# Kernel tuning notes

Hardware: AMD Instinct MI355X
Metric: run time of the kernel (lower is better)

## Reference

```python
import jax, jax.numpy as jnp
import numpy as np

DIM = 25
N_NODES = 20000
N_EDGES = 320000
NFEAT = 300
NHID = 64
NCLASS = 50


def setup_inputs() -> dict:
    key = jax.random.key(0)
    ks = jax.random.split(key, 8)
    s1 = np.sqrt(6.0 / (NFEAT + NHID))
    s2 = np.sqrt(6.0 / (NHID * DIM + NCLASS))
    return {
        "x": jax.random.normal(ks[0], (N_NODES, NFEAT), dtype=jnp.float32),
        "adj_rows": jax.random.randint(ks[1], (DIM, N_EDGES), 0, N_NODES, dtype=jnp.int32),
        "adj_cols": jax.random.randint(ks[2], (DIM, N_EDGES), 0, N_NODES, dtype=jnp.int32),
        "adj_vals": jax.random.uniform(ks[3], (DIM, N_EDGES), dtype=jnp.float32),
        "W1": jax.random.uniform(ks[4], (DIM, NFEAT, NHID), dtype=jnp.float32, minval=-s1, maxval=s1),
        "b1": jnp.zeros((DIM, NHID), dtype=jnp.float32),
        "W2": jax.random.uniform(ks[5], (DIM, NHID * DIM, NCLASS), dtype=jnp.float32, minval=-s2, maxval=s2),
        "b2": jnp.zeros((DIM, NCLASS), dtype=jnp.float32),
    }


def _spmm(rows, cols, vals, sup, n):
    # sparse [n,n] @ dense [n,f] via gather + segment-sum scatter-add
    return jax.ops.segment_sum(vals[:, None] * sup[cols], rows, num_segments=n)


def reference(x, adj_rows, adj_cols, adj_vals, W1, b1, W2, b2):
    n = x.shape[0]
    spmm = jax.vmap(lambda r, c, v, s: _spmm(r, c, v, s, n))
    # layer 1: per-branch dense mm, spmm, bias, relu  -> [DIM, n, NHID]
    sup1 = jnp.einsum("nf,dfh->dnh", x, W1)
    h1 = jax.nn.relu(spmm(adj_rows, adj_cols, adj_vals, sup1) + b1[:, None, :])
    # permute + reshape: concat branch features per node -> [n, DIM*NHID]
    h1cat = jnp.transpose(h1, (1, 0, 2)).reshape(n, -1)
    # layer 2: per-branch dense mm, spmm, bias, relu -> [DIM, n, NCLASS]
    sup2 = jnp.einsum("nk,dkc->dnc", h1cat, W2)
    h2 = jax.nn.relu(spmm(adj_rows, adj_cols, adj_vals, sup2) + b2[:, None, :])
    # max-pool over branches (POOLING='max')
    return jnp.max(h2, axis=0)
```

## Files before the change

### kernel.cpp

```cpp
#include <hip/hip_runtime.h>
#include <hip/hip_bf16.h>
#include <cstdint>
#include <cstddef>

#define DIM 25
#define NN 20000
#define NE 320000
#define NF 300
#define NH 64
#define NC 50
#define K2 (DIM*NH)
#define KP1 320
#define B1T_ROWS 1664
#define B2T_ROWS 1280
#define NBK 79
#define EPB 4096
#define BPB ((NE + EPB - 1) / EPB)
#define FCAP 5632

typedef __attribute__((ext_vector_type(8))) short short8;
typedef __attribute__((ext_vector_type(4))) float floatx4;
typedef __hip_bfloat16 bf16;

static __device__ __forceinline__ unsigned bf16bits(float f) {
    bf16 b = __float2bfloat16(f);
    return (unsigned)*reinterpret_cast<unsigned short*>(&b);
}
static __device__ __forceinline__ float blo(unsigned w) { return __uint_as_float(w << 16); }
static __device__ __forceinline__ float bhi(unsigned w) { return __uint_as_float(w & 0xFFFF0000u); }

static __device__ __forceinline__ void gld16(const void* g, void* l) {
    __builtin_amdgcn_global_load_lds((const __attribute__((address_space(1))) unsigned*)g,
                                     (__attribute__((address_space(3))) unsigned*)l, 16, 0, 0);
}

__global__ void zero_kernel(int* __restrict__ p, int n) {
    int i = blockIdx.x * blockDim.x + threadIdx.x;
    if (i < n) p[i] = 0;
}

__global__ __launch_bounds__(256) void bucket_scatter_kernel(const int* __restrict__ rows,
                                                             const int* __restrict__ cols,
                                                             const float* __restrict__ vals,
                                                             int* __restrict__ gcur,
                                                             unsigned* __restrict__ interE,
                                                             unsigned char* __restrict__ interR) {
    const int d = blockIdx.y;
    const int e0 = blockIdx.x * EPB;
    __shared__ int lh[NBK];
    __shared__ int lo[NBK];
    __shared__ int lbase[NBK];
    __shared__ unsigned entE[EPB];
    __shared__ unsigned short entR[EPB];
    const int tid = threadIdx.x;
    for (int i = tid; i < NBK; i += 256) lh[i] = 0;
    __syncthreads();
    const int* rd = rows + (size_t)d * NE;
    const int* cd = cols + (size_t)d * NE;
    const float* vd = vals + (size_t)d * NE;
    const int e1 = min(e0 + EPB, NE);
    const int ne = e1 - e0;
    for (int i = e0 + tid; i < e1; i += 256)
        atomicAdd(&lh[rd[i] >> 8], 1);
    __syncthreads();
    if (tid == 0) {
        int run = 0;
        for (int b = 0; b < NBK; ++b) { lo[b] = run; run += lh[b]; }
    }
    __syncthreads();
    for (int i = tid; i < NBK; i += 256) {
        lbase[i] = lh[i] ? atomicAdd(&gcur[d * NBK + i], lh[i]) : 0;
        lh[i] = 0;
    }
    __syncthreads();
    for (int i = e0 + tid; i < e1; i += 256) {
        int r = rd[i];
        int b = r >> 8;
        int rank = atomicAdd(&lh[b], 1);
        int pos = lo[b] + rank;
        entE[pos] = (unsigned)cd[i] | (bf16bits(vd[i]) << 16);
        entR[pos] = (unsigned short)r;
    }
    __syncthreads();
    for (int p = tid; p < ne; p += 256) {
        int r = entR[p];
        int b = r >> 8;
        int gpos = lbase[b] + (p - lo[b]);
        if (gpos < FCAP) {
            size_t slot = ((size_t)d * NBK + b) * FCAP + gpos;
            interE[slot] = entE[p];
            interR[slot] = (unsigned char)r;
        }
    }
}

__global__ void bucket_scan_kernel(const int* __restrict__ gcur,
                                   int* __restrict__ offs_b,
                                   int* __restrict__ bcnt,
                                   int* __restrict__ offs) {
    const int d = blockIdx.x;
    if (threadIdx.x != 0) return;
    int run = 0;
    for (int b = 0; b < NBK; ++b) {
        int c = min(gcur[d * NBK + b], FCAP);
        offs_b[d * NBK + b] = run;
        bcnt[d * NBK + b] = c;
        run += c;
    }
    offs[d * (NN + 1) + NN] = run;
}

__global__ __launch_bounds__(256) void csr_finalize_kernel(const unsigned* __restrict__ interE,
                                                           const unsigned char* __restrict__ interR,
                                                           const int* __restrict__ offs_b,
                                                           const int* __restrict__ bcnt,
                                                           int* __restrict__ offs,
                                                           unsigned* __restrict__ sedge) {
    const int d = blockIdx.y;
    const int b = blockIdx.x;
    const int tid = threadIdx.x;
    const int s = offs_b[d * NBK + b];
    const int cnt = bcnt[d * NBK + b];
    const size_t base = ((size_t)d * NBK + b) * FCAP;
    __shared__ int sm[256];
    __shared__ int cur[256];
    __shared__ unsigned lse[FCAP];
    sm[tid] = 0;
    __syncthreads();
    for (int i = tid; i < cnt; i += 256)
        atomicAdd(&sm[interR[base + i]], 1);
    __syncthreads();
    int own = sm[tid];
    for (int off = 1; off < 256; off <<= 1) {
        int t = (tid >= off) ? sm[tid - off] : 0;
        __syncthreads();
        sm[tid] += t;
        __syncthreads();
    }
    int excl = sm[tid] - own;
    int row = (b << 8) + tid;
    if (row < NN) offs[d * (NN + 1) + row] = s + excl;
    cur[tid] = excl;
    __syncthreads();
    for (int i = tid; i < cnt; i += 256) {
        int idx = atomicAdd(&cur[interR[base + i]], 1);
        lse[idx] = interE[base + i];
    }
    __syncthreads();
    unsigned* sed = sedge + (size_t)d * NE;
    for (int t = tid; t < cnt; t += 256)
        sed[s + t] = lse[t];
}

__global__ void pack_x_kernel(const float* __restrict__ x, bf16* __restrict__ xb) {
    int i = blockIdx.x * blockDim.x + threadIdx.x;
    if (i >= NN * KP1) return;
    int n = i / KP1, k = i - n * KP1;
    xb[i] = __float2bfloat16((k < NF) ? x[(size_t)n * NF + k] : 0.f);
}

__global__ void pack_b1_kernel(const float* __restrict__ W1, bf16* __restrict__ b1t) {
    int i = blockIdx.x * blockDim.x + threadIdx.x;
    if (i >= B1T_ROWS * KP1) return;
    int j2 = i / KP1, k = i - j2 * KP1;
    int chunk = j2 >> 9;
    int r = j2 & 511;
    int d = chunk * 8 + (r >> 6);
    float v = 0.f;
    if (d < DIM && k < NF)
        v = W1[(size_t)d * NF * NH + (size_t)k * NH + (r & 63)];
    b1t[i] = __float2bfloat16(v);
}

__global__ void pack_b2_kernel(const float* __restrict__ W2, bf16* __restrict__ b2t) {
    int i = blockIdx.x * blockDim.x + threadIdx.x;
    if (i >= B2T_ROWS * K2) return;
    int r = i / K2, k = i - r * K2;
    float v = 0.f;
    if (r < DIM * NC) {
        int g = r / NC, c = r - g * NC;
        v = W2[(size_t)g * K2 * NC + (size_t)k * NC + c];
    }
    b2t[i] = __float2bfloat16(v);
}

__global__ __launch_bounds__(256) void gemm_bf16_kernel(const bf16* __restrict__ A, int lda,
                                                        const bf16* __restrict__ BT, int ldb,
                                                        bf16* __restrict__ C,
                                                        int ksteps, int mode, int nvalid) {
    __shared__ unsigned short As[3 * 128 * 32];
    __shared__ unsigned short Bs[3 * 128 * 32];
    const int tid = threadIdx.x;
    const int wave = tid >> 6;
    const int lane = tid & 63;

    const int mtiles = (int)gridDim.x;
    const int ntiles = (int)gridDim.y;
    const int bid = (int)blockIdx.y * mtiles + (int)blockIdx.x;
    const int per_group = 8 * ntiles;
    const int group = bid / per_group;
    const int rem = bid - group * per_group;
    const int first_m = group * 8;
    const int gm = min(8, mtiles - first_m);
    const int mt = first_m + rem % gm;
    const int nt = rem / gm;
    const int m0 = mt * 128;
    const int n0 = nt * 128;

    const int wm = (wave >> 1) * 64;
    const int wn = (wave & 1) * 64;
    floatx4 acc[4][4] = {};
    const int r0 = tid >> 2;
    const int cg = (tid & 3) ^ ((r0 >> 1) & 3);
    const int q8 = (lane >> 4) * 8;
    const int gq = q8 >> 3;
    unsigned short* lA0 = As + wave * 512;
    unsigned short* lA1 = As + 2048 + wave * 512;
    unsigned short* lB0 = Bs + wave * 512;
    unsigned short* lB1 = Bs + 2048 + wave * 512;
    const bf16* gA0 = A + (size_t)(m0 + r0) * lda + cg * 8;
    const bf16* gA1 = A + (size_t)(m0 + r0 + 64) * lda + cg * 8;
    const bf16* gB0 = BT + (size_t)(n0 + r0) * ldb + cg * 8;
    const bf16* gB1 = BT + (size_t)(n0 + r0 + 64) * ldb + cg * 8;

    int offA[4], offB[4];
    #pragma unroll
    for (int i = 0; i < 4; ++i) {
        int ra = wm + i * 16 + (lane & 15);
        int rb = wn + i * 16 + (lane & 15);
        offA[i] = ra * 32 + ((gq ^ ((ra >> 1) & 3)) << 3);
        offB[i] = rb * 32 + ((gq ^ ((rb >> 1) & 3)) << 3);
    }

    gld16(gA0, lA0); gld16(gA1, lA1); gld16(gB0, lB0); gld16(gB1, lB1);
    if (ksteps > 1) {
        gld16(gA0 + 32, lA0 + 4096); gld16(gA1 + 32, lA1 + 4096);
        gld16(gB0 + 32, lB0 + 4096); gld16(gB1 + 32, lB1 + 4096);
    }
    const bf16* pA0 = gA0 + 64;
    const bf16* pA1 = gA1 + 64;
    const bf16* pB0 = gB0 + 64;
    const bf16* pB1 = gB1 + 64;

    int buf = 0;
    int pbuf = 2;
    for (int ks = 0; ks < ksteps; ++ks) {
        if (ks + 1 < ksteps) asm volatile("s_waitcnt vmcnt(4)" ::: "memory");
        else                 asm volatile("s_waitcnt vmcnt(0)" ::: "memory");
        __builtin_amdgcn_sched_barrier(0);
        __builtin_amdgcn_s_barrier();
        __builtin_amdgcn_sched_barrier(0);
        if (ks + 2 < ksteps) {
            unsigned short* dA0 = lA0 + pbuf * 4096;
            unsigned short* dA1 = lA1 + pbuf * 4096;
            unsigned short* dB0 = lB0 + pbuf * 4096;
            unsigned short* dB1 = lB1 + pbuf * 4096;
            gld16(pA0, dA0); gld16(pA1, dA1); gld16(pB0, dB0); gld16(pB1, dB1);
            pA0 += 32; pA1 += 32; pB0 += 32; pB1 += 32;
            pbuf = (pbuf == 2) ? 0 : pbuf + 1;
        }
        const unsigned short* as = As + buf * 4096;
        const unsigned short* bs = Bs + buf * 4096;
        short8 af[4], bfr[4];
        #pragma unroll
        for (int i = 0; i < 4; ++i) {
            af[i]  = *(const short8*)&as[offA[i]];
            bfr[i] = *(const short8*)&bs[offB[i]];
        }
        #pragma unroll
        for (int i = 0; i < 4; ++i)
            #pragma unroll
            for (int j = 0; j < 4; ++j)
                acc[i][j] = __builtin_amdgcn_mfma_f32_16x16x32_bf16(af[i], bfr[j], acc[i][j], 0, 0, 0);
        buf = (buf == 2) ? 0 : buf + 1;
    }
    const int cr = (lane >> 4) * 4;
    const int cc = lane & 15;
    #pragma unroll
    for (int i = 0; i < 4; ++i) {
        #pragma unroll
        for (int r = 0; r < 4; ++r) {
            int m = m0 + wm + i * 16 + cr + r;
            if (m >= NN) continue;
            #pragma unroll
            for (int j = 0; j < 4; ++j) {
                int n = n0 + wn + j * 16 + cc;
                if (n >= nvalid) continue;
                if (mode == 1) {
                    int g = n >> 6, h = n & 63;
                    C[(size_t)g * NN * NH + (size_t)m * NH + h] = __float2bfloat16(acc[i][j][r]);
                } else {
                    int g = n / NC, c = n - g * NC;
                    C[(size_t)g * NN * NC + (size_t)m * NC + c] = __float2bfloat16(acc[i][j][r]);
                }
            }
        }
    }
}

__global__ __launch_bounds__(256) void spmm1_kernel(const bf16* __restrict__ sup,
                                                    const int* __restrict__ offs,
                                                    const unsigned* __restrict__ sedge,
                                                    const float* __restrict__ b1,
                                                    bf16* __restrict__ h1cat, int d0, int CHk) {
    const int i = blockIdx.x;
    const int g = i % CHk;
    const int nb = i / CHk;
    const int tid = threadIdx.x;
    const int lane = tid & 63;
    const int n = nb * 8 + ((tid >> 6) << 1) + (lane >> 5);
    const int hl = lane & 31;
    const int d = d0 + g;
    const int s = offs[d * (NN + 1) + n];
    const int e = offs[d * (NN + 1) + n + 1];
    const char* supd = (const char*)sup + (size_t)g * NN * NH * 2;
    const unsigned* sed = sedge + (size_t)d * NE;
    const unsigned hoff = (unsigned)hl * 4;
    float alo0 = 0.f, ahi0 = 0.f, alo1 = 0.f, ahi1 = 0.f;
    int j = s;
    for (; j + 4 <= e; j += 4) {
        unsigned e0 = sed[j], e1 = sed[j + 1], e2 = sed[j + 2], e3 = sed[j + 3];
        unsigned w0 = *(const unsigned*)(supd + (((e0 & 0xFFFFu) << 7) | hoff));
        unsigned w1 = *(const unsigned*)(supd + (((e1 & 0xFFFFu) << 7) | hoff));
        unsigned w2 = *(const unsigned*)(supd + (((e2 & 0xFFFFu) << 7) | hoff));
        unsigned w3 = *(const unsigned*)(supd + (((e3 & 0xFFFFu) << 7) | hoff));
        float v0 = bhi(e0), v1 = bhi(e1), v2 = bhi(e2), v3 = bhi(e3);
        alo0 = fmaf(v0, blo(w0), alo0); ahi0 = fmaf(v0, bhi(w0), ahi0);
        alo1 = fmaf(v1, blo(w1), alo1); ahi1 = fmaf(v1, bhi(w1), ahi1);
        alo0 = fmaf(v2, blo(w2), alo0); ahi0 = fmaf(v2, bhi(w2), ahi0);
        alo1 = fmaf(v3, blo(w3), alo1); ahi1 = fmaf(v3, bhi(w3), ahi1);
    }
    for (; j < e; ++j) {
        unsigned e0 = sed[j];
        unsigned w0 = *(const unsigned*)(supd + (((e0 & 0xFFFFu) << 7) | hoff));
        float v0 = bhi(e0);
        alo0 = fmaf(v0, blo(w0), alo0); ahi0 = fmaf(v0, bhi(w0), ahi0);
    }
    float alo = fmaxf((alo0 + alo1) + b1[d * NH + 2 * hl], 0.f);
    float ahi = fmaxf((ahi0 + ahi1) + b1[d * NH + 2 * hl + 1], 0.f);
    unsigned packed = bf16bits(alo) | (bf16bits(ahi) << 16);
    *(unsigned*)((char*)h1cat + ((size_t)n * K2 + d * NH) * 2 + hoff) = packed;
}

__global__ __launch_bounds__(256) void spmm2b_kernel(const bf16* __restrict__ sup2,
                                                     const int* __restrict__ offs,
                                                     const unsigned* __restrict__ sedge,
                                                     const float* __restrict__ b2,
                                                     unsigned* __restrict__ h2u) {
    const int i = blockIdx.x;
    const int r = i & 7;
    const int q = i >> 3;
    int d, nb;
    if (q < 7500) { d = r + 8 * (q / 2500); nb = q % 2500; }
    else { d = 24; nb = (q - 7500) * 8 + r; if (nb >= 2500) return; }
    const int tid = threadIdx.x;
    const int lane = tid & 63;
    const int n = nb * 8 + ((tid >> 6) << 1) + (lane >> 5);
    const int cl = min(lane & 31, 24);
    const unsigned coff = (unsigned)cl * 4;
    const int s = offs[d * (NN + 1) + n];
    const int e = offs[d * (NN + 1) + n + 1];
    const char* supd = (const char*)sup2 + (size_t)d * NN * NC * 2;
    const unsigned* sed = sedge + (size_t)d * NE;
    float alo0 = b2[d * NC + 2 * cl], ahi0 = b2[d * NC + 2 * cl + 1];
    float alo1 = 0.f, ahi1 = 0.f;
    int j = s;
    for (; j + 4 <= e; j += 4) {
        unsigned e0 = sed[j], e1 = sed[j + 1], e2 = sed[j + 2], e3 = sed[j + 3];
        unsigned w0 = *(const unsigned*)(supd + ((e0 & 0xFFFFu) * 100u + coff));
        unsigned w1 = *(const unsigned*)(supd + ((e1 & 0xFFFFu) * 100u + coff));
        unsigned w2 = *(const unsigned*)(supd + ((e2 & 0xFFFFu) * 100u + coff));
        unsigned w3 = *(const unsigned*)(supd + ((e3 & 0xFFFFu) * 100u + coff));
        float v0 = bhi(e0), v1 = bhi(e1), v2 = bhi(e2), v3 = bhi(e3);
        alo0 = fmaf(v0, blo(w0), alo0); ahi0 = fmaf(v0, bhi(w0), ahi0);
        alo1 = fmaf(v1, blo(w1), alo1); ahi1 = fmaf(v1, bhi(w1), ahi1);
        alo0 = fmaf(v2, blo(w2), alo0); ahi0 = fmaf(v2, bhi(w2), ahi0);
        alo1 = fmaf(v3, blo(w3), alo1); ahi1 = fmaf(v3, bhi(w3), ahi1);
    }
    for (; j < e; ++j) {
        unsigned e0 = sed[j];
        unsigned w0 = *(const unsigned*)(supd + ((e0 & 0xFFFFu) * 100u + coff));
        float v0 = bhi(e0);
        alo0 = fmaf(v0, blo(w0), alo0); ahi0 = fmaf(v0, bhi(w0), ahi0);
    }
    float alo = fmaxf(alo0 + alo1, 0.f);
    float ahi = fmaxf(ahi0 + ahi1, 0.f);
    if ((lane & 31) < 25)
        h2u[((size_t)d * NN + n) * 25 + cl] = bf16bits(alo) | (bf16bits(ahi) << 16);
}

__global__ __launch_bounds__(256) void maxk_kernel(const unsigned* __restrict__ h2u,
                                                   float* __restrict__ out) {
    int i = blockIdx.x * blockDim.x + threadIdx.x;
    if (i >= NN * 25) return;
    int n = i / 25, cl = i - n * 25;
    float mlo = 0.f, mhi = 0.f;
    #pragma unroll
    for (int d = 0; d < DIM; ++d) {
        unsigned w = h2u[(size_t)d * NN * 25 + i];
        mlo = fmaxf(mlo, blo(w));
        mhi = fmaxf(mhi, bhi(w));
    }
    *(float2*)&out[(size_t)n * NC + 2 * cl] = make_float2(mlo, mhi);
}

extern "C" void kernel_launch(void* const* d_in, const int* in_sizes, int n_in,
                              void* d_out, int out_size, void* d_ws, size_t ws_size,
                              hipStream_t stream) {
    const float* x    = (const float*)d_in[0];
    const int*   rows = (const int*)d_in[1];
    const int*   cols = (const int*)d_in[2];
    const float* vals = (const float*)d_in[3];
    const float* W1   = (const float*)d_in[4];
    const float* b1   = (const float*)d_in[5];
    const float* W2   = (const float*)d_in[6];
    const float* b2   = (const float*)d_in[7];
    float* out = (float*)d_out;

    char* ws = (char*)d_ws;
    size_t off = 0;
    auto alloc = [&](size_t bytes) {
        void* p = ws + off;
        off += (bytes + 255) & ~(size_t)255;
        return p;
    };
    bf16* supbuf = (bf16*)alloc(sizeof(bf16) * (size_t)DIM * NN * NC);
    bf16* h1cat  = (bf16*)alloc(sizeof(bf16) * (size_t)NN * K2);
    bf16* b1t    = (bf16*)alloc(sizeof(bf16) * (size_t)B1T_ROWS * KP1);
    bf16* b2t    = (bf16*)alloc(sizeof(bf16) * (size_t)B2T_ROWS * K2);
    int*  offs   = (int*)alloc(sizeof(int) * (size_t)DIM * (NN + 1));
    int*  gcur   = (int*)alloc(sizeof(int) * (size_t)DIM * NBK);
    int*  offs_b = (int*)alloc(sizeof(int) * (size_t)DIM * NBK);
    int*  bcnt   = (int*)alloc(sizeof(int) * (size_t)DIM * NBK);
    unsigned* sedge = (unsigned*)alloc(sizeof(unsigned) * (size_t)DIM * NE);

    bf16* sup1 = supbuf;
    bf16* xbf  = supbuf + (size_t)12 * 1024 * 1024;
    bf16* sup2 = supbuf;
    unsigned* interE = (unsigned*)h1cat;
    unsigned char* interR = (unsigned char*)h1cat + (size_t)DIM * NBK * FCAP * 4;
    unsigned* h2u = (unsigned*)h1cat;

    if (off > ws_size) return;

    zero_kernel<<<(DIM * NBK + 255) / 256, 256, 0, stream>>>(gcur, DIM * NBK);
    bucket_scatter_kernel<<<dim3(BPB, DIM), 256, 0, stream>>>(rows, cols, vals, gcur, interE, interR);
    bucket_scan_kernel<<<DIM, 64, 0, stream>>>(gcur, offs_b, bcnt, offs);
    csr_finalize_kernel<<<dim3(NBK, DIM), 256, 0, stream>>>(interE, interR, offs_b, bcnt, offs, sedge);

    pack_x_kernel<<<(NN * KP1 + 255) / 256, 256, 0, stream>>>(x, xbf);
    pack_b1_kernel<<<(B1T_ROWS * KP1 + 255) / 256, 256, 0, stream>>>(W1, b1t);
    pack_b2_kernel<<<(B2T_ROWS * K2 + 255) / 256, 256, 0, stream>>>(W2, b2t);

    const int mtiles = (NN + 127) / 128;

    const int cstart[4] = {0, 8, 16, 24};
    const int csize[4]  = {8, 8, 8, 1};
    const int crow[4]   = {0, 512, 1024, 1536};
    for (int c = 0; c < 4; ++c) {
        int nv = csize[c] * 64;
        gemm_bf16_kernel<<<dim3(mtiles, (nv + 127) / 128), 256, 0, stream>>>(
            xbf, KP1, b1t + (size_t)crow[c] * KP1, KP1, sup1, KP1 / 32, 1, nv);
        spmm1_kernel<<<csize[c] * (NN / 8), 256, 0, stream>>>(
            sup1, offs, sedge, b1, h1cat, cstart[c], csize[c]);
    }
    gemm_bf16_kernel<<<dim3(mtiles, B2T_ROWS / 128), 256, 0, stream>>>(
        h1cat, K2, b2t, K2, sup2, K2 / 32, 2, DIM * NC);
    spmm2b_kernel<<<8 * 7813, 256, 0, stream>>>(sup2, offs, sedge, b2, h2u);
    maxk_kernel<<<(NN * 25 + 255) / 256, 256, 0, stream>>>(h2u, out);
}
```

Baseline: 755.5 us.

## Add 256x256-tile bf16 MFMA GEMM kernel for layer-1 chunks and layer-2

Adds a 512-thread GEMM kernel with 256x256 output tiles, 64-wide K tiles, double-buffered LDS filled by global_load_lds, inline-asm ds_read_b128 fragment loads and s_setprio around MFMA bursts. It replaces the 128x128 GEMM for the three full layer-1 branch chunks and for the layer-2 GEMM, while the last single-branch layer-1 chunk keeps the old kernel. The aim is more data reuse per LDS load and fewer K-loop barriers. In exchange, each block uses about 128 KB of LDS, so only one block fits per CU. The grids also get much smaller (158 blocks for layer 1), which may leave CUs idle or cause a tail.

```diff
diff --git a/kernel.cpp b/kernel.cpp
--- a/kernel.cpp
+++ b/kernel.cpp
@@ -33,6 +33,10 @@
     __builtin_amdgcn_global_load_lds((const __attribute__((address_space(1))) unsigned*)g,
                                      (__attribute__((address_space(3))) unsigned*)l, 16, 0, 0);
 }
+static __device__ __forceinline__ unsigned lds_off(const void* p) {
+    return (unsigned)(size_t)(const __attribute__((address_space(3))) char*)p;
+}
+#define DSR(dst, a, off) asm volatile("ds_read_b128 %0, %1 offset:" #off : "=v"(dst) : "v"(a))
 
 __global__ void zero_kernel(int* __restrict__ p, int n) {
     int i = blockIdx.x * blockDim.x + threadIdx.x;
@@ -184,6 +188,164 @@
     b2t[i] = __float2bfloat16(v);
 }
 
+__global__ __launch_bounds__(512, 2) void gemm256_bf16_kernel(const bf16* __restrict__ A, int lda,
+                                                              const bf16* __restrict__ BT, int ldb,
+                                                              bf16* __restrict__ C,
+                                                              int ktiles, int mode, int nvalid) {
+    __shared__ unsigned short As[2 * 256 * 64];
+    __shared__ unsigned short Bs[2 * 256 * 64];
+    const int tid = threadIdx.x;
+    const int w = tid >> 6;
+    const int l = tid & 63;
+    const int MT = (int)gridDim.x;
+    const int NT = (int)gridDim.y;
+    const int bid = (int)blockIdx.y * MT + (int)blockIdx.x;
+    const int pg = 8 * NT;
+    const int grp = bid / pg;
+    const int rem = bid - grp * pg;
+    const int fm = grp * 8;
+    const int gm = min(8, MT - fm);
+    const int mt = fm + rem % gm;
+    const int nt = rem / gm;
+    const int m0 = mt * 256, n0 = nt * 256;
+    const int wr = w >> 2, wc = w & 3;
+
+    floatx4 acc[8][4] = {};
+
+    const int strow = w * 8 + (l >> 3);
+    const int gch = (l & 7) ^ (l >> 3);
+    const bf16* pA[4];
+    const bf16* pB[4];
+    #pragma unroll
+    for (int q = 0; q < 4; ++q) {
+        pA[q] = A + (size_t)(m0 + q * 64 + strow) * lda + gch * 8;
+        pB[q] = BT + (size_t)(n0 + q * 64 + strow) * ldb + gch * 8;
+    }
+    const unsigned slc0 = (unsigned)(((l >> 4)) ^ (l & 7)) * 16u;
+    const unsigned slc1 = (unsigned)((4 + (l >> 4)) ^ (l & 7)) * 16u;
+    const unsigned aRow = (unsigned)(wr * 128 + (l & 15)) * 128u;
+    const unsigned bRow = (unsigned)(wc * 64 + (l & 15)) * 128u;
+    const unsigned ldsA = lds_off(As), ldsB = lds_off(Bs);
+
+    #pragma unroll
+    for (int q = 0; q < 4; ++q) { gld16(pA[q], As + q * 4096 + w * 512); pA[q] += 64; }
+    #pragma unroll
+    for (int q = 0; q < 4; ++q) { gld16(pB[q], Bs + q * 4096 + w * 512); pB[q] += 64; }
+    asm volatile("s_waitcnt vmcnt(0)");
+    __builtin_amdgcn_sched_barrier(0);
+    __builtin_amdgcn_s_barrier();
+    __builtin_amdgcn_sched_barrier(0);
+
+    short8 aF[4][2], bF[4][2];
+    for (int kt = 0; kt < ktiles; ++kt) {
+        const int c = kt & 1;
+        const unsigned boff = (unsigned)c * 32768u;
+        const unsigned aA0 = ldsA + boff + aRow + slc0;
+        const unsigned aA1 = ldsA + boff + aRow + slc1;
+        const unsigned bA0 = ldsB + boff + bRow + slc0;
+        const unsigned bA1 = ldsB + boff + bRow + slc1;
+        unsigned short* nA = As + (c ^ 1) * 16384 + w * 512;
+        unsigned short* nB = Bs + (c ^ 1) * 16384 + w * 512;
+        const bool stage = (kt + 1 < ktiles);
+        DSR(aF[0][0], aA0, 0);    DSR(aF[0][1], aA1, 0);
+        DSR(aF[1][0], aA0, 2048); DSR(aF[1][1], aA1, 2048);
+        DSR(aF[2][0], aA0, 4096); DSR(aF[2][1], aA1, 4096);
+        DSR(aF[3][0], aA0, 6144); DSR(aF[3][1], aA1, 6144);
+        DSR(bF[0][0], bA0, 0);    DSR(bF[0][1], bA1, 0);
+        DSR(bF[1][0], bA0, 2048); DSR(bF[1][1], bA1, 2048);
+        if (stage) {
+            gld16(pA[0], nA);         gld16(pA[1], nA + 4096);
+            gld16(pA[2], nA + 8192);  gld16(pA[3], nA + 12288);
+            pA[0] += 64; pA[1] += 64; pA[2] += 64; pA[3] += 64;
+        }
+        asm volatile("s_waitcnt lgkmcnt(0)");
+        __builtin_amdgcn_sched_barrier(0);
+        __builtin_amdgcn_s_setprio(1);
+        #pragma unroll
+        for (int mf = 0; mf < 4; ++mf)
+            #pragma unroll
+            for (int nf = 0; nf < 2; ++nf) {
+                acc[mf][nf] = __builtin_amdgcn_mfma_f32_16x16x32_bf16(aF[mf][0], bF[nf][0], acc[mf][nf], 0, 0, 0);
+                acc[mf][nf] = __builtin_amdgcn_mfma_f32_16x16x32_bf16(aF[mf][1], bF[nf][1], acc[mf][nf], 0, 0, 0);
+            }
+        __builtin_amdgcn_s_setprio(0);
+        __builtin_amdgcn_sched_barrier(0);
+        DSR(bF[2][0], bA0, 4096); DSR(bF[2][1], bA1, 4096);
+        DSR(bF[3][0], bA0, 6144); DSR(bF[3][1], bA1, 6144);
+        if (stage) {
+            gld16(pB[0], nB);         gld16(pB[1], nB + 4096);
+            gld16(pB[2], nB + 8192);  gld16(pB[3], nB + 12288);
+            pB[0] += 64; pB[1] += 64; pB[2] += 64; pB[3] += 64;
+        }
+        asm volatile("s_waitcnt lgkmcnt(0)");
+        __builtin_amdgcn_sched_barrier(0);
+        __builtin_amdgcn_s_setprio(1);
+        #pragma unroll
+        for (int mf = 0; mf < 4; ++mf)
+            #pragma unroll
+            for (int nf = 2; nf < 4; ++nf) {
+                acc[mf][nf] = __builtin_amdgcn_mfma_f32_16x16x32_bf16(aF[mf][0], bF[nf][0], acc[mf][nf], 0, 0, 0);
+                acc[mf][nf] = __builtin_amdgcn_mfma_f32_16x16x32_bf16(aF[mf][1], bF[nf][1], acc[mf][nf], 0, 0, 0);
+            }
+        __builtin_amdgcn_s_setprio(0);
+        __builtin_amdgcn_sched_barrier(0);
+        DSR(aF[0][0], aA0, 8192);  DSR(aF[0][1], aA1, 8192);
+        DSR(aF[1][0], aA0, 10240); DSR(aF[1][1], aA1, 10240);
+        DSR(aF[2][0], aA0, 12288); DSR(aF[2][1], aA1, 12288);
+        DSR(aF[3][0], aA0, 14336); DSR(aF[3][1], aA1, 14336);
+        asm volatile("s_waitcnt lgkmcnt(0)");
+        __builtin_amdgcn_sched_barrier(0);
+        __builtin_amdgcn_s_setprio(1);
+        #pragma unroll
+        for (int mf = 0; mf < 4; ++mf)
+            #pragma unroll
+            for (int nf = 2; nf < 4; ++nf) {
+                acc[mf + 4][nf] = __builtin_amdgcn_mfma_f32_16x16x32_bf16(aF[mf][0], bF[nf][0], acc[mf + 4][nf], 0, 0, 0);
+                acc[mf + 4][nf] = __builtin_amdgcn_mfma_f32_16x16x32_bf16(aF[mf][1], bF[nf][1], acc[mf + 4][nf], 0, 0, 0);
+            }
+        __builtin_amdgcn_s_setprio(0);
+        __builtin_amdgcn_sched_barrier(0);
+        __builtin_amdgcn_s_setprio(1);
+        #pragma unroll
+        for (int mf = 0; mf < 4; ++mf)
+            #pragma unroll
+            for (int nf = 0; nf < 2; ++nf) {
+                acc[mf + 4][nf] = __builtin_amdgcn_mfma_f32_16x16x32_bf16(aF[mf][0], bF[nf][0], acc[mf + 4][nf], 0, 0, 0);
+                acc[mf + 4][nf] = __builtin_amdgcn_mfma_f32_16x16x32_bf16(aF[mf][1], bF[nf][1], acc[mf + 4][nf], 0, 0, 0);
+            }
+        __builtin_amdgcn_s_setprio(0);
+        __builtin_amdgcn_sched_barrier(0);
+        if (stage) {
+            asm volatile("s_waitcnt vmcnt(0)");
+            __builtin_amdgcn_sched_barrier(0);
+            __builtin_amdgcn_s_barrier();
+            __builtin_amdgcn_sched_barrier(0);
+        }
+    }
+    const int cr = (l >> 4) * 4;
+    const int cc = l & 15;
+    #pragma unroll
+    for (int mf = 0; mf < 8; ++mf) {
+        #pragma unroll
+        for (int r = 0; r < 4; ++r) {
+            int m = m0 + wr * 128 + mf * 16 + cr + r;
+            if (m >= NN) continue;
+            #pragma unroll
+            for (int nf = 0; nf < 4; ++nf) {
+                int n = n0 + wc * 64 + nf * 16 + cc;
+                if (n >= nvalid) continue;
+                if (mode == 1) {
+                    int g = n >> 6, h = n & 63;
+                    C[(size_t)g * NN * NH + (size_t)m * NH + h] = __float2bfloat16(acc[mf][nf][r]);
+                } else {
+                    int g = n / NC, cl2 = n - g * NC;
+                    C[(size_t)g * NN * NC + (size_t)m * NC + cl2] = __float2bfloat16(acc[mf][nf][r]);
+                }
+            }
+        }
+    }
+}
+
 __global__ __launch_bounds__(256) void gemm_bf16_kernel(const bf16* __restrict__ A, int lda,
                                                         const bf16* __restrict__ BT, int ldb,
                                                         bf16* __restrict__ C,
@@ -193,7 +355,6 @@
     const int tid = threadIdx.x;
     const int wave = tid >> 6;
     const int lane = tid & 63;
-
     const int mtiles = (int)gridDim.x;
     const int ntiles = (int)gridDim.y;
     const int bid = (int)blockIdx.y * mtiles + (int)blockIdx.x;
@@ -206,7 +367,6 @@
     const int nt = rem / gm;
     const int m0 = mt * 128;
     const int n0 = nt * 128;
-
     const int wm = (wave >> 1) * 64;
     const int wn = (wave & 1) * 64;
     floatx4 acc[4][4] = {};
@@ -222,7 +382,6 @@
     const bf16* gA1 = A + (size_t)(m0 + r0 + 64) * lda + cg * 8;
     const bf16* gB0 = BT + (size_t)(n0 + r0) * ldb + cg * 8;
     const bf16* gB1 = BT + (size_t)(n0 + r0 + 64) * ldb + cg * 8;
-
     int offA[4], offB[4];
     #pragma unroll
     for (int i = 0; i < 4; ++i) {
@@ -231,7 +390,6 @@
         offA[i] = ra * 32 + ((gq ^ ((ra >> 1) & 3)) << 3);
         offB[i] = rb * 32 + ((gq ^ ((rb >> 1) & 3)) << 3);
     }
-
     gld16(gA0, lA0); gld16(gA1, lA1); gld16(gB0, lB0); gld16(gB1, lB1);
     if (ksteps > 1) {
         gld16(gA0 + 32, lA0 + 4096); gld16(gA1 + 32, lA1 + 4096);
@@ -241,7 +399,6 @@
     const bf16* pA1 = gA1 + 64;
     const bf16* pB0 = gB0 + 64;
     const bf16* pB1 = gB1 + 64;
-
     int buf = 0;
     int pbuf = 2;
     for (int ks = 0; ks < ksteps; ++ks) {
@@ -452,20 +609,25 @@
     pack_b1_kernel<<<(B1T_ROWS * KP1 + 255) / 256, 256, 0, stream>>>(W1, b1t);
     pack_b2_kernel<<<(B2T_ROWS * K2 + 255) / 256, 256, 0, stream>>>(W2, b2t);
 
-    const int mtiles = (NN + 127) / 128;
+    const int mtiles128 = (NN + 127) / 128;
+    const int mtiles256 = (NN + 255) / 256;
 
     const int cstart[4] = {0, 8, 16, 24};
     const int csize[4]  = {8, 8, 8, 1};
     const int crow[4]   = {0, 512, 1024, 1536};
-    for (int c = 0; c < 4; ++c) {
-        int nv = csize[c] * 64;
-        gemm_bf16_kernel<<<dim3(mtiles, (nv + 127) / 128), 256, 0, stream>>>(
-            xbf, KP1, b1t + (size_t)crow[c] * KP1, KP1, sup1, KP1 / 32, 1, nv);
+    for (int c = 0; c < 3; ++c) {
+        gemm256_bf16_kernel<<<dim3(mtiles256, 2), 512, 0, stream>>>(
+            xbf, KP1, b1t + (size_t)crow[c] * KP1, KP1, sup1, KP1 / 64, 1, 512);
         spmm1_kernel<<<csize[c] * (NN / 8), 256, 0, stream>>>(
             sup1, offs, sedge, b1, h1cat, cstart[c], csize[c]);
     }
-    gemm_bf16_kernel<<<dim3(mtiles, B2T_ROWS / 128), 256, 0, stream>>>(
-        h1cat, K2, b2t, K2, sup2, K2 / 32, 2, DIM * NC);
+    gemm_bf16_kernel<<<dim3(mtiles128, 1), 256, 0, stream>>>(
+        xbf, KP1, b1t + (size_t)crow[3] * KP1, KP1, sup1, KP1 / 32, 1, 64);
+    spmm1_kernel<<<csize[3] * (NN / 8), 256, 0, stream>>>(
+        sup1, offs, sedge, b1, h1cat, cstart[3], csize[3]);
+
+    gemm256_bf16_kernel<<<dim3(mtiles256, B2T_ROWS / 256), 512, 0, stream>>>(
+        h1cat, K2, b2t, K2, sup2, K2 / 64, 2, DIM * NC);
     spmm2b_kernel<<<8 * 7813, 256, 0, stream>>>(sup2, offs, sedge, b2, h2u);
     maxk_kernel<<<(NN * 25 + 255) / 256, 256, 0, stream>>>(h2u, out);
 }
```

After: 727.8 us. 1.04x faster.
